# Performance work log

Hardware: AMD Instinct MI355X
Metric: run time of the kernel (lower is better)

## Reference

```python
import jax, jax.numpy as jnp
import numpy as np
from jax import lax

N, GH, GE, LH, LL = 19, 64, 64, 64, 2
B, T = 256, 256


def _normalized_adjacency(A):
    # A: (..., n, n). Add self-loops, symmetric degree normalization.
    n = A.shape[-1]
    A = A + jnp.eye(n, dtype=A.dtype)
    deg = jnp.clip(A.sum(axis=-1), 1e-6, None)  # (..., n)
    dis = deg ** -0.5
    return A * dis[..., :, None] * dis[..., None, :]


def _graph_encoder(A, w1_w, w1_b, w2_w, w2_b):
    # A: (B, T, n, n) -> (B, T, GE). Node features X = A rows.
    An = _normalized_adjacency(A)
    X = jax.nn.relu(An @ (A @ w1_w.T + w1_b))   # (B,T,n,GH)
    X = jax.nn.relu(An @ (X @ w2_w.T + w2_b))   # (B,T,n,GE)
    return X.mean(axis=-2)


def _lstm_layer(x, Wih, Whh, bih, bhh):
    # x: (B, T, D); PyTorch gate order i,f,g,o. Returns (B, T, H).
    Bb = x.shape[0]
    H = Whh.shape[1]
    xg = x @ Wih.T + (bih + bhh)  # precompute input contributions (B,T,4H)

    def step(carry, xt):
        h, c = carry
        gates = xt + h @ Whh.T
        i, f, g, o = jnp.split(gates, 4, axis=-1)
        c = jax.nn.sigmoid(f) * c + jax.nn.sigmoid(i) * jnp.tanh(g)
        h = jax.nn.sigmoid(o) * jnp.tanh(c)
        return (h, c), h

    h0 = jnp.zeros((Bb, H), x.dtype)
    (_, _), hs = lax.scan(step, (h0, h0), jnp.swapaxes(xg, 0, 1))
    return jnp.swapaxes(hs, 0, 1)


def setup_inputs() -> dict:
    key = jax.random.key(0)
    ks = jax.random.split(key, 20)
    s = 0.1
    inp = {
        'conn': jax.random.uniform(ks[0], (B, T, N, N), jnp.float32),
        'mask': jnp.ones((B, T), jnp.int32),
        'w1_w': jax.random.normal(ks[1], (GH, N), jnp.float32) * s,
        'w1_b': jax.random.normal(ks[2], (GH,), jnp.float32) * s,
        'w2_w': jax.random.normal(ks[3], (GE, GH), jnp.float32) * s,
        'w2_b': jax.random.normal(ks[4], (GE,), jnp.float32) * s,
        'lstm_Wih0': jax.random.normal(ks[5], (4 * LH, GE), jnp.float32) * s,
        'lstm_Whh0': jax.random.normal(ks[6], (4 * LH, LH), jnp.float32) * s,
        'lstm_bih0': jax.random.normal(ks[7], (4 * LH,), jnp.float32) * s,
        'lstm_bhh0': jax.random.normal(ks[8], (4 * LH,), jnp.float32) * s,
        'lstm_Wih1': jax.random.normal(ks[9], (4 * LH, LH), jnp.float32) * s,
        'lstm_Whh1': jax.random.normal(ks[10], (4 * LH, LH), jnp.float32) * s,
        'lstm_bih1': jax.random.normal(ks[11], (4 * LH,), jnp.float32) * s,
        'lstm_bhh1': jax.random.normal(ks[12], (4 * LH,), jnp.float32) * s,
        'fc1_w': jax.random.normal(ks[13], (32, LH), jnp.float32) * s,
        'fc1_b': jax.random.normal(ks[14], (32,), jnp.float32) * s,
        'fc2_w': jax.random.normal(ks[15], (2, 32), jnp.float32) * s,
        'fc2_b': jax.random.normal(ks[16], (2,), jnp.float32) * s,
    }
    return inp


def reference(conn, mask, w1_w, w1_b, w2_w, w2_b,
              lstm_Wih0, lstm_Whh0, lstm_bih0, lstm_bhh0,
              lstm_Wih1, lstm_Whh1, lstm_bih1, lstm_bhh1,
              fc1_w, fc1_b, fc2_w, fc2_b):
    emb = _graph_encoder(conn, w1_w, w1_b, w2_w, w2_b)  # (B,T,GE)
    mf = mask.astype(emb.dtype)
    emb = emb * mf[:, :, None]
    out = _lstm_layer(emb, lstm_Wih0, lstm_Whh0, lstm_bih0, lstm_bhh0)
    out = _lstm_layer(out, lstm_Wih1, lstm_Whh1, lstm_bih1, lstm_bhh1)  # (B,T,LH)
    lengths = jnp.clip(mask.sum(axis=1), 1, None)
    last_idx = jnp.clip(lengths - 1, 0, None)  # (B,)
    last_h = jnp.take_along_axis(out, last_idx[:, None, None], axis=1)[:, 0, :]
    h = jax.nn.relu(last_h @ fc1_w.T + fc1_b)
    return h @ fc2_w.T + fc2_b  # (B,2) logits
```

## Files before the change

### kernel.cpp

```cpp
#include <hip/hip_runtime.h>
#include <hip/hip_bf16.h>
#include <math.h>

#define GN 19
#define BB 256
#define TT 256

typedef short short8 __attribute__((ext_vector_type(8)));
typedef float f4 __attribute__((ext_vector_type(4)));
typedef unsigned short u16;

union Frag { int i[4]; short8 s; };

#define LWAIT() __asm__ volatile("s_waitcnt lgkmcnt(0)" ::: "memory")
#define WGBAR() __asm__ volatile("s_waitcnt lgkmcnt(0)\ns_barrier" ::: "memory")
#define PIN8(x) __asm__ volatile("" : "+v"(x))
#define PINF(x) __asm__ volatile("" : "+v"(x))

#define MFMA(a,b,c) __builtin_amdgcn_mfma_f32_16x16x32_bf16(a,b,c,0,0,0)

__device__ __forceinline__ int pkbf(float a, float b) {
    __hip_bfloat162 h2 = __float22bfloat162_rn(make_float2(a, b));
    union { __hip_bfloat162 h; int i; } u; u.h = h2; return u.i;
}

__device__ __forceinline__ float fexp2(float x) { return __builtin_amdgcn_exp2f(x); }
__device__ __forceinline__ float frcp(float x)  { return __builtin_amdgcn_rcpf(x); }
__device__ __forceinline__ float sigm(float x)  { return frcp(1.f + fexp2(-1.4426950408889634f * x)); }
__device__ __forceinline__ float tanha(float x) { float e = fexp2(2.8853900817779268f * x); return 1.f - 2.f * frcp(e + 1.f); }

__global__ __launch_bounds__(64) void encoder_mfma(
    const float* __restrict__ conn,
    const int*   __restrict__ mask,
    const float* __restrict__ w1_w,
    const float* __restrict__ w1_b,
    const float* __restrict__ w2_w,
    const float* __restrict__ w2_b,
    u16* __restrict__ emb,
    int num_graphs)
{
    __shared__ float S[2304];
    __shared__ float dis[32];
    __shared__ float ps[256];

    const int t = threadIdx.x;
    const int l15 = t & 15;
    const int quad = t >> 4;

    float km[8];
    #pragma unroll
    for (int j = 0; j < 8; ++j) km[j] = (quad * 8 + j < GN) ? 1.f : 0.f;

    int rr[6], cc[6];
    #pragma unroll
    for (int i = 0; i < 6; ++i) {
        int e = t + 64 * i;
        rr[i] = e / GN;
        cc[i] = e - rr[i] * GN;
    }

    Frag w1F[4];
    #pragma unroll
    for (int nt = 0; nt < 4; ++nt) {
        int n = nt * 16 + l15;
        #pragma unroll
        for (int p = 0; p < 4; ++p) {
            int k0 = quad * 8 + 2 * p, k1 = k0 + 1;
            float a = (k0 < GN) ? w1_w[n * GN + k0] : 0.f;
            float b = (k1 < GN) ? w1_w[n * GN + k1] : 0.f;
            w1F[nt].i[p] = pkbf(a, b);
        }
    }
    Frag w2F[2][4];
    #pragma unroll
    for (int kt = 0; kt < 2; ++kt)
        #pragma unroll
        for (int nt = 0; nt < 4; ++nt) {
            int n = nt * 16 + l15;
            #pragma unroll
            for (int p = 0; p < 4; ++p) {
                int k = kt * 32 + quad * 8 + 2 * p;
                w2F[kt][nt].i[p] = pkbf(w2_w[n * 64 + k], w2_w[n * 64 + k + 1]);
            }
        }
    float b1v[4], b2v[4];
    #pragma unroll
    for (int nt = 0; nt < 4; ++nt) {
        b1v[nt] = w1_b[nt * 16 + l15];
        b2v[nt] = w2_b[nt * 16 + l15];
    }

    float pf[6];
    {
        int g0 = blockIdx.x < num_graphs ? blockIdx.x : 0;
        const float* Ag = conn + (size_t)g0 * (GN * GN);
        #pragma unroll
        for (int i = 0; i < 6; ++i) {
            int e = t + 64 * i;
            if (e < GN * GN) pf[i] = Ag[e];
        }
    }

    #pragma unroll 1
    for (int g = blockIdx.x; g < num_graphs; g += gridDim.x) {
        #pragma unroll
        for (int i = 0; i < 4; ++i) {
            int s = t + 64 * i;
            int row = s >> 3, c4 = s & 7;
            f4 z = {0.f, 0.f, 0.f, 0.f};
            *(f4*)&S[row * 68 + c4 * 4] = z;
        }
        LWAIT();
        #pragma unroll
        for (int i = 0; i < 6; ++i) {
            if (t + 64 * i < GN * GN) S[rr[i] * 68 + cc[i]] = pf[i];
        }
        {
            int gn = g + gridDim.x;
            const float* Ag = conn + (size_t)(gn < num_graphs ? gn : g) * (GN * GN);
            #pragma unroll
            for (int i = 0; i < 6; ++i) {
                int e = t + 64 * i;
                if (e < GN * GN) pf[i] = Ag[e];
            }
        }
        LWAIT();

        if (t < 32) {
            float dv = 0.f;
            if (t < GN) {
                float d = 1.0f;
                #pragma unroll
                for (int c4 = 0; c4 < 8; ++c4) {
                    f4 v = *(f4*)&S[t * 68 + c4 * 4];
                    d += v.x + v.y + v.z + v.w;
                }
                dv = rsqrtf(d);
            }
            dis[t] = dv;
        }
        LWAIT();

        float dk[8];
        {
            f4 v0 = *(f4*)&dis[quad * 8];
            f4 v1 = *(f4*)&dis[quad * 8 + 4];
            dk[0]=v0.x; dk[1]=v0.y; dk[2]=v0.z; dk[3]=v0.w;
            dk[4]=v1.x; dk[5]=v1.y; dk[6]=v1.z; dk[7]=v1.w;
        }
        Frag aF[2], anF[2];
        #pragma unroll
        for (int mt = 0; mt < 2; ++mt) {
            int m = l15 + 16 * mt;
            float dm = dis[m];
            f4 v0 = *(f4*)&S[m * 68 + quad * 8];
            f4 v1 = *(f4*)&S[m * 68 + quad * 8 + 4];
            float av[8] = {v0.x, v0.y, v0.z, v0.w, v1.x, v1.y, v1.z, v1.w};
            float an[8];
            #pragma unroll
            for (int j = 0; j < 8; ++j) {
                int k = quad * 8 + j;
                an[j] = (av[j] + (m == k ? 1.f : 0.f)) * dm * dk[j];
            }
            #pragma unroll
            for (int p = 0; p < 4; ++p) {
                aF[mt].i[p]  = pkbf(av[2*p], av[2*p+1]);
                anF[mt].i[p] = pkbf(an[2*p], an[2*p+1]);
            }
        }
        LWAIT();

        #pragma unroll
        for (int mt = 0; mt < 2; ++mt)
            #pragma unroll
            for (int nt = 0; nt < 4; ++nt) {
                float bb = b1v[nt];
                f4 c = {bb, bb, bb, bb};
                c = MFMA(aF[mt].s, w1F[nt].s, c);
                int col = nt * 16 + l15;
                #pragma unroll
                for (int r = 0; r < 4; ++r)
                    S[col * 36 + (mt * 16 + quad * 4 + r)] = c[r];
            }
        LWAIT();

        Frag hF[4];
        #pragma unroll
        for (int nt = 0; nt < 4; ++nt) {
            int n = nt * 16 + l15;
            f4 v0 = *(f4*)&S[n * 36 + quad * 8];
            f4 v1 = *(f4*)&S[n * 36 + quad * 8 + 4];
            float vv[8] = {v0.x, v0.y, v0.z, v0.w, v1.x, v1.y, v1.z, v1.w};
            #pragma unroll
            for (int p = 0; p < 4; ++p)
                hF[nt].i[p] = pkbf(vv[2*p] * km[2*p], vv[2*p+1] * km[2*p+1]);
        }
        LWAIT();

        #pragma unroll
        for (int mt = 0; mt < 2; ++mt)
            #pragma unroll
            for (int nt = 0; nt < 4; ++nt) {
                f4 c = {0.f, 0.f, 0.f, 0.f};
                c = MFMA(anF[mt].s, hF[nt].s, c);
                int col = nt * 16 + l15;
                #pragma unroll
                for (int r = 0; r < 4; ++r)
                    S[(mt * 16 + quad * 4 + r) * 68 + col] = fmaxf(c[r], 0.f);
            }
        LWAIT();

        Frag xF[2][2];
        #pragma unroll
        for (int mt = 0; mt < 2; ++mt) {
            int m = l15 + 16 * mt;
            #pragma unroll
            for (int kt = 0; kt < 2; ++kt) {
                f4 v0 = *(f4*)&S[m * 68 + kt * 32 + quad * 8];
                f4 v1 = *(f4*)&S[m * 68 + kt * 32 + quad * 8 + 4];
                xF[mt][kt].i[0] = pkbf(v0.x, v0.y);
                xF[mt][kt].i[1] = pkbf(v0.z, v0.w);
                xF[mt][kt].i[2] = pkbf(v1.x, v1.y);
                xF[mt][kt].i[3] = pkbf(v1.z, v1.w);
            }
        }
        LWAIT();

        #pragma unroll
        for (int mt = 0; mt < 2; ++mt)
            #pragma unroll
            for (int nt = 0; nt < 4; ++nt) {
                float bb = b2v[nt];
                f4 c = {bb, bb, bb, bb};
                c = MFMA(xF[mt][0].s, w2F[0][nt].s, c);
                c = MFMA(xF[mt][1].s, w2F[1][nt].s, c);
                int col = nt * 16 + l15;
                #pragma unroll
                for (int r = 0; r < 4; ++r)
                    S[col * 36 + (mt * 16 + quad * 4 + r)] = c[r];
            }
        LWAIT();

        Frag hG[4];
        #pragma unroll
        for (int nt = 0; nt < 4; ++nt) {
            int n = nt * 16 + l15;
            f4 v0 = *(f4*)&S[n * 36 + quad * 8];
            f4 v1 = *(f4*)&S[n * 36 + quad * 8 + 4];
            float vv[8] = {v0.x, v0.y, v0.z, v0.w, v1.x, v1.y, v1.z, v1.w};
            #pragma unroll
            for (int p = 0; p < 4; ++p)
                hG[nt].i[p] = pkbf(vv[2*p] * km[2*p], vv[2*p+1] * km[2*p+1]);
        }

        float cs[4];
        #pragma unroll
        for (int nt = 0; nt < 4; ++nt) cs[nt] = 0.f;
        #pragma unroll
        for (int mt = 0; mt < 2; ++mt)
            #pragma unroll
            for (int nt = 0; nt < 4; ++nt) {
                f4 c = {0.f, 0.f, 0.f, 0.f};
                c = MFMA(anF[mt].s, hG[nt].s, c);
                if (mt == 0) {
                    cs[nt] += fmaxf(c[0], 0.f) + fmaxf(c[1], 0.f)
                            + fmaxf(c[2], 0.f) + fmaxf(c[3], 0.f);
                } else if (quad == 0) {
                    cs[nt] += fmaxf(c[0], 0.f) + fmaxf(c[1], 0.f) + fmaxf(c[2], 0.f);
                }
            }
        #pragma unroll
        for (int nt = 0; nt < 4; ++nt)
            ps[quad * 64 + nt * 16 + l15] = cs[nt];
        LWAIT();
        float tot = ps[t] + ps[64 + t] + ps[128 + t] + ps[192 + t];
        float mf = (float)mask[g];
        float v = tot * (1.f / 19.f) * mf;
        emb[(size_t)g * 64 + t] = (u16)(unsigned)pkbf(v, v);
        LWAIT();
    }
}

__device__ __forceinline__ void read_h1(const u16* __restrict__ hs,
                                        int off, Frag* __restrict__ BH)
{
    #pragma unroll
    for (int kt = 0; kt < 2; ++kt) {
        int4 vh = *(const int4*)&hs[off + kt * 32];
        BH[kt].i[0] = vh.x; BH[kt].i[1] = vh.y;
        BH[kt].i[2] = vh.z; BH[kt].i[3] = vh.w;
    }
}

__global__ __launch_bounds__(512) __attribute__((amdgpu_waves_per_eu(2, 2)))
void lstm_mfma(
    const u16*   __restrict__ x,
    const int*   __restrict__ mask,
    const float* __restrict__ Wih0, const float* __restrict__ Whh0,
    const float* __restrict__ bih0, const float* __restrict__ bhh0,
    const float* __restrict__ Wih1, const float* __restrict__ Whh1,
    const float* __restrict__ bih1, const float* __restrict__ bhh1,
    const float* __restrict__ fc1_w, const float* __restrict__ fc1_b,
    const float* __restrict__ fc2_w, const float* __restrict__ fc2_b,
    float* __restrict__ out)
{
    __shared__ __attribute__((aligned(16))) u16 h0s[2][16 * 72];
    __shared__ __attribute__((aligned(16))) u16 h1s[2][16 * 72];
    __shared__ float hlast[16][68];
    __shared__ float red[512];
    __shared__ int   li_s[16];

    const int tid  = threadIdx.x;
    const int w    = tid >> 6;
    const int grp  = w >> 2;
    const int wl   = w & 3;
    const int lane = tid & 63;
    const int l15  = lane & 15;
    const int quad = lane >> 4;
    const int bb0  = blockIdx.x * 16;

    for (int i = tid; i < 16 * 72; i += 512) h1s[0][i] = 0;

    {
        int b16 = tid >> 5, j = tid & 31;
        int s = 0;
        #pragma unroll
        for (int c8 = 0; c8 < 8; ++c8)
            s += mask[(bb0 + b16) * TT + j + 32 * c8];
        red[tid] = (float)s;
    }
    __syncthreads();
    if (tid < 16) {
        float s = 0.f;
        #pragma unroll
        for (int j = 0; j < 32; ++j) s += red[tid * 32 + j];
        int li = (int)s - 1;
        li_s[tid] = li < 0 ? 0 : (li > TT - 1 ? TT - 1 : li);
    }
    __syncthreads();
    const int li = li_s[l15];

    const float* __restrict__ Wx = grp ? Wih1 : Wih0;
    const float* __restrict__ Wh = grp ? Whh1 : Whh0;
    const float* __restrict__ bi = grp ? bih1 : bih0;
    const float* __restrict__ bh = grp ? bhh1 : bhh0;

    Frag Ax[4][2], Ah[4][2];
    f4 biasv[4];
    #pragma unroll
    for (int mt = 0; mt < 4; ++mt) {
        int mg = 4 * wl + mt;
        int orig = (l15 & 3) * 64 + (mg * 4 + (l15 >> 2));
        #pragma unroll
        for (int kt = 0; kt < 2; ++kt)
            #pragma unroll
            for (int p = 0; p < 4; ++p) {
                int k = kt * 32 + quad * 8 + 2 * p;
                Ax[mt][kt].i[p] = pkbf(Wx[orig * 64 + k], Wx[orig * 64 + k + 1]);
                Ah[mt][kt].i[p] = pkbf(Wh[orig * 64 + k], Wh[orig * 64 + k + 1]);
            }
        int uu = mg * 4 + quad;
        #pragma unroll
        for (int r = 0; r < 4; ++r)
            biasv[mt][r] = bi[r * 64 + uu] + bh[r * 64 + uu];
    }
    #pragma unroll
    for (int mt = 0; mt < 4; ++mt) {
        PIN8(Ax[mt][0].s); PIN8(Ax[mt][1].s);
        PIN8(Ah[mt][0].s); PIN8(Ah[mt][1].s);
        PINF(biasv[mt]);
    }

    const int ubase = 16 * wl + quad;
    const int hoff = l15 * 72 + quad * 8;

    Frag BH0[2], BH1[2], BXn[2];
    #pragma unroll
    for (int kt = 0; kt < 2; ++kt)
        #pragma unroll
        for (int p = 0; p < 4; ++p) {
            BXn[kt].i[p] = 0; BH0[kt].i[p] = 0; BH1[kt].i[p] = 0;
        }
    float cst[4] = {0.f, 0.f, 0.f, 0.f};
    float hlv[4] = {0.f, 0.f, 0.f, 0.f};

    const u16* __restrict__ xb = x + (size_t)(bb0 + l15) * TT * 64;
    if (grp == 0) {
        BXn[0] = *(const Frag*)&xb[quad * 8];
        BXn[1] = *(const Frag*)&xb[32 + quad * 8];
    }

    #pragma unroll 1
    for (int it = 0; it <= TT; ++it) {
        const int cur = it & 1;
        f4 g[4];
        bool act = false;

        if (grp == 0) {
            if (it < TT) {
                act = true;
                Frag bx0 = BXn[0], bx1 = BXn[1];
                int tn = it + 1 < TT ? it + 1 : TT - 1;
                BXn[0] = *(const Frag*)&xb[(size_t)tn * 64 + quad * 8];
                BXn[1] = *(const Frag*)&xb[(size_t)tn * 64 + 32 + quad * 8];

                #pragma unroll
                for (int mt = 0; mt < 4; ++mt) {
                    f4 ca = biasv[mt];
                    ca = MFMA(Ax[mt][0].s, bx0.s,    ca);
                    ca = MFMA(Ah[mt][0].s, BH0[0].s, ca);
                    f4 cb = {0.f, 0.f, 0.f, 0.f};
                    cb = MFMA(Ax[mt][1].s, bx1.s,    cb);
                    cb = MFMA(Ah[mt][1].s, BH0[1].s, cb);
                    g[mt] = ca + cb;
                }
            }
        } else {
            if (it >= 1) {
                act = true;
                #pragma unroll
                for (int mt = 0; mt < 4; ++mt) {
                    f4 ca = biasv[mt];
                    ca = MFMA(Ax[mt][0].s, BH0[0].s, ca);
                    ca = MFMA(Ah[mt][0].s, BH1[0].s, ca);
                    f4 cb = {0.f, 0.f, 0.f, 0.f};
                    cb = MFMA(Ax[mt][1].s, BH0[1].s, cb);
                    cb = MFMA(Ah[mt][1].s, BH1[1].s, cb);
                    g[mt] = ca + cb;
                }
            }
        }

        if (act) {
            u16* __restrict__ dst = grp ? h1s[cur] : h0s[cur];
            #pragma unroll
            for (int mt = 0; mt < 4; ++mt) {
                f4 gg = g[mt];
                float si = sigm(gg[0]), sf = sigm(gg[1]);
                float tg = tanha(gg[2]), so = sigm(gg[3]);
                float cc = fmaf(sf, cst[mt], si * tg);
                cst[mt] = cc;
                float h = so * tanha(cc);
                if (grp && it - 1 == li) hlv[mt] = h;
                dst[l15 * 72 + ubase + 4 * mt] = (u16)(unsigned)pkbf(h, h);
            }
        }

        WGBAR();

        if (it < TT) {
            read_h1(h0s[cur], hoff, BH0);
            if (grp) read_h1(h1s[cur], hoff, BH1);
        }
    }

    if (grp == 1) {
        #pragma unroll
        for (int mt = 0; mt < 4; ++mt)
            hlast[l15][ubase + 4 * mt] = hlv[mt];
    }
    __syncthreads();
    {
        int b = tid >> 5, o = tid & 31;
        float acc = fc1_b[o];
        const float* fw = fc1_w + o * 64;
        #pragma unroll
        for (int j = 0; j < 64; ++j)
            acc = fmaf(hlast[b][j], fw[j], acc);
        red[b * 32 + o] = fmaxf(acc, 0.f);
    }
    __syncthreads();
    if (tid < 32) {
        int b = tid >> 1, o = tid & 1;
        float acc = fc2_b[o];
        #pragma unroll
        for (int j = 0; j < 32; ++j)
            acc = fmaf(fc2_w[o * 32 + j], red[b * 32 + j], acc);
        out[(bb0 + b) * 2 + o] = acc;
    }
}

extern "C" void kernel_launch(void* const* d_in, const int* in_sizes, int n_in,
                              void* d_out, int out_size, void* d_ws, size_t ws_size,
                              hipStream_t stream)
{
    const float* conn  = (const float*)d_in[0];
    const int*   mask  = (const int*)  d_in[1];
    const float* w1_w  = (const float*)d_in[2];
    const float* w1_b  = (const float*)d_in[3];
    const float* w2_w  = (const float*)d_in[4];
    const float* w2_b  = (const float*)d_in[5];
    const float* Wih0  = (const float*)d_in[6];
    const float* Whh0  = (const float*)d_in[7];
    const float* bih0  = (const float*)d_in[8];
    const float* bhh0  = (const float*)d_in[9];
    const float* Wih1  = (const float*)d_in[10];
    const float* Whh1  = (const float*)d_in[11];
    const float* bih1  = (const float*)d_in[12];
    const float* bhh1  = (const float*)d_in[13];
    const float* fc1_w = (const float*)d_in[14];
    const float* fc1_b = (const float*)d_in[15];
    const float* fc2_w = (const float*)d_in[16];
    const float* fc2_b = (const float*)d_in[17];

    float* out = (float*)d_out;
    u16*   emb = (u16*)d_ws;

    const int num_graphs = BB * TT;

    encoder_mfma<<<8192, 64, 0, stream>>>(
        conn, mask, w1_w, w1_b, w2_w, w2_b, emb, num_graphs);

    lstm_mfma<<<16, 512, 0, stream>>>(
        emb, mask, Wih0, Whh0, bih0, bhh0, Wih1, Whh1, bih1, bhh1,
        fc1_w, fc1_b, fc2_w, fc2_b, out);
}
```

Measured before the change: 539.9 us.

## Pack four graph waves per encoder block with shared bf16 weight fragments

The encoder now runs 256-thread blocks with four independent waves, each handling its own graph stream, and keeps the pre-packed bf16 weight fragments in LDS instead of per-thread registers. Intermediate activations are stored in LDS as bf16 with a smaller per-wave footprint, so the pack/convert steps between MFMAs disappear. The final mean reduction uses cross-lane shuffles instead of an LDS scratch buffer. The intent is to cut register pressure and LDS use, raise occupancy and reduce LDS traffic, at the cost of extra LDS reads of weights on every graph.

```diff
diff --git a/kernel.cpp b/kernel.cpp
--- a/kernel.cpp
+++ b/kernel.cpp
@@ -23,13 +23,17 @@
     __hip_bfloat162 h2 = __float22bfloat162_rn(make_float2(a, b));
     union { __hip_bfloat162 h; int i; } u; u.h = h2; return u.i;
 }
+__device__ __forceinline__ u16 bf16of(float v) {
+    return (u16)(unsigned)pkbf(v, v);
+}
 
 __device__ __forceinline__ float fexp2(float x) { return __builtin_amdgcn_exp2f(x); }
 __device__ __forceinline__ float frcp(float x)  { return __builtin_amdgcn_rcpf(x); }
 __device__ __forceinline__ float sigm(float x)  { return frcp(1.f + fexp2(-1.4426950408889634f * x)); }
 __device__ __forceinline__ float tanha(float x) { float e = fexp2(2.8853900817779268f * x); return 1.f - 2.f * frcp(e + 1.f); }
 
-__global__ __launch_bounds__(64) void encoder_mfma(
+__global__ __launch_bounds__(256) __attribute__((amdgpu_waves_per_eu(2, 4)))
+void encoder_mfma(
     const float* __restrict__ conn,
     const int*   __restrict__ mask,
     const float* __restrict__ w1_w,
@@ -39,17 +43,56 @@
     u16* __restrict__ emb,
     int num_graphs)
 {
-    __shared__ float S[2304];
-    __shared__ float dis[32];
-    __shared__ float ps[256];
-
-    const int t = threadIdx.x;
+    __shared__ __attribute__((aligned(16))) float SA[4][1280];
+    __shared__ __attribute__((aligned(16))) u16  wb[12][64][8];
+    __shared__ float dis4[4][32];
+
+    const int tid = threadIdx.x;
+    const int tw  = tid >> 6;
+    const int t   = tid & 63;
     const int l15 = t & 15;
     const int quad = t >> 4;
 
-    float km[8];
+    if (tw == 0) {
+        #pragma unroll
+        for (int nt = 0; nt < 4; ++nt) {
+            int n = nt * 16 + l15;
+            Frag f;
+            #pragma unroll
+            for (int p = 0; p < 4; ++p) {
+                int k0 = quad * 8 + 2 * p, k1 = k0 + 1;
+                float a = (k0 < GN) ? w1_w[n * GN + k0] : 0.f;
+                float b = (k1 < GN) ? w1_w[n * GN + k1] : 0.f;
+                f.i[p] = pkbf(a, b);
+            }
+            *(int4*)&wb[nt][t][0] = *(int4*)&f;
+        }
+        #pragma unroll
+        for (int kt = 0; kt < 2; ++kt)
+            #pragma unroll
+            for (int nt = 0; nt < 4; ++nt) {
+                int n = nt * 16 + l15;
+                Frag f;
+                #pragma unroll
+                for (int p = 0; p < 4; ++p) {
+                    int k = kt * 32 + quad * 8 + 2 * p;
+                    f.i[p] = pkbf(w2_w[n * 64 + k], w2_w[n * 64 + k + 1]);
+                }
+                *(int4*)&wb[4 + kt * 4 + nt][t][0] = *(int4*)&f;
+            }
+    }
+    float b1v[4], b2v[4];
     #pragma unroll
-    for (int j = 0; j < 8; ++j) km[j] = (quad * 8 + j < GN) ? 1.f : 0.f;
+    for (int nt = 0; nt < 4; ++nt) {
+        b1v[nt] = w1_b[nt * 16 + l15];
+        b2v[nt] = w2_b[nt * 16 + l15];
+    }
+    __syncthreads();
+
+    float* __restrict__ S   = SA[tw];
+    u16*  __restrict__ SH   = (u16*)S;
+    u16*  __restrict__ SX   = (u16*)S;
+    float* __restrict__ dis = dis4[tw];
 
     int rr[6], cc[6];
     #pragma unroll
@@ -59,40 +102,9 @@
         cc[i] = e - rr[i] * GN;
     }
 
-    Frag w1F[4];
-    #pragma unroll
-    for (int nt = 0; nt < 4; ++nt) {
-        int n = nt * 16 + l15;
-        #pragma unroll
-        for (int p = 0; p < 4; ++p) {
-            int k0 = quad * 8 + 2 * p, k1 = k0 + 1;
-            float a = (k0 < GN) ? w1_w[n * GN + k0] : 0.f;
-            float b = (k1 < GN) ? w1_w[n * GN + k1] : 0.f;
-            w1F[nt].i[p] = pkbf(a, b);
-        }
-    }
-    Frag w2F[2][4];
-    #pragma unroll
-    for (int kt = 0; kt < 2; ++kt)
-        #pragma unroll
-        for (int nt = 0; nt < 4; ++nt) {
-            int n = nt * 16 + l15;
-            #pragma unroll
-            for (int p = 0; p < 4; ++p) {
-                int k = kt * 32 + quad * 8 + 2 * p;
-                w2F[kt][nt].i[p] = pkbf(w2_w[n * 64 + k], w2_w[n * 64 + k + 1]);
-            }
-        }
-    float b1v[4], b2v[4];
-    #pragma unroll
-    for (int nt = 0; nt < 4; ++nt) {
-        b1v[nt] = w1_b[nt * 16 + l15];
-        b2v[nt] = w2_b[nt * 16 + l15];
-    }
-
     float pf[6];
     {
-        int g0 = blockIdx.x < num_graphs ? blockIdx.x : 0;
+        int g0 = blockIdx.x * 4 + tw;
         const float* Ag = conn + (size_t)g0 * (GN * GN);
         #pragma unroll
         for (int i = 0; i < 6; ++i) {
@@ -102,21 +114,21 @@
     }
 
     #pragma unroll 1
-    for (int g = blockIdx.x; g < num_graphs; g += gridDim.x) {
+    for (int g = blockIdx.x * 4 + tw; g < num_graphs; g += gridDim.x * 4) {
         #pragma unroll
         for (int i = 0; i < 4; ++i) {
             int s = t + 64 * i;
             int row = s >> 3, c4 = s & 7;
             f4 z = {0.f, 0.f, 0.f, 0.f};
-            *(f4*)&S[row * 68 + c4 * 4] = z;
+            *(f4*)&S[row * 36 + c4 * 4] = z;
         }
         LWAIT();
         #pragma unroll
         for (int i = 0; i < 6; ++i) {
-            if (t + 64 * i < GN * GN) S[rr[i] * 68 + cc[i]] = pf[i];
+            if (t + 64 * i < GN * GN) S[rr[i] * 36 + cc[i]] = pf[i];
         }
         {
-            int gn = g + gridDim.x;
+            int gn = g + gridDim.x * 4;
             const float* Ag = conn + (size_t)(gn < num_graphs ? gn : g) * (GN * GN);
             #pragma unroll
             for (int i = 0; i < 6; ++i) {
@@ -132,7 +144,7 @@
                 float d = 1.0f;
                 #pragma unroll
                 for (int c4 = 0; c4 < 8; ++c4) {
-                    f4 v = *(f4*)&S[t * 68 + c4 * 4];
+                    f4 v = *(f4*)&S[t * 36 + c4 * 4];
                     d += v.x + v.y + v.z + v.w;
                 }
                 dv = rsqrtf(d);
@@ -153,8 +165,8 @@
         for (int mt = 0; mt < 2; ++mt) {
             int m = l15 + 16 * mt;
             float dm = dis[m];
-            f4 v0 = *(f4*)&S[m * 68 + quad * 8];
-            f4 v1 = *(f4*)&S[m * 68 + quad * 8 + 4];
+            f4 v0 = *(f4*)&S[m * 36 + quad * 8];
+            f4 v1 = *(f4*)&S[m * 36 + quad * 8 + 4];
             float av[8] = {v0.x, v0.y, v0.z, v0.w, v1.x, v1.y, v1.z, v1.w};
             float an[8];
             #pragma unroll
@@ -171,43 +183,45 @@
         LWAIT();
 
         #pragma unroll
-        for (int mt = 0; mt < 2; ++mt)
-            #pragma unroll
-            for (int nt = 0; nt < 4; ++nt) {
+        for (int nt = 0; nt < 4; ++nt) {
+            Frag wf; *(int4*)&wf = *(int4*)&wb[nt][t][0];
+            int nn = nt * 16 + l15;
+            #pragma unroll
+            for (int mt = 0; mt < 2; ++mt) {
                 float bb = b1v[nt];
                 f4 c = {bb, bb, bb, bb};
-                c = MFMA(aF[mt].s, w1F[nt].s, c);
-                int col = nt * 16 + l15;
-                #pragma unroll
-                for (int r = 0; r < 4; ++r)
-                    S[col * 36 + (mt * 16 + quad * 4 + r)] = c[r];
-            }
+                c = MFMA(aF[mt].s, wf.s, c);
+                #pragma unroll
+                for (int r = 0; r < 4; ++r) {
+                    int k = mt * 16 + quad * 4 + r;
+                    float vv = c[r];
+                    if (mt == 1) vv = (quad == 0 && r < 3) ? vv : 0.f;
+                    SH[nn * 40 + k] = bf16of(vv);
+                }
+            }
+        }
         LWAIT();
 
         Frag hF[4];
         #pragma unroll
+        for (int nt = 0; nt < 4; ++nt)
+            *(int4*)&hF[nt] = *(const int4*)&SH[(nt * 16 + l15) * 40 + quad * 8];
+        LWAIT();
+
+        #pragma unroll
         for (int nt = 0; nt < 4; ++nt) {
-            int n = nt * 16 + l15;
-            f4 v0 = *(f4*)&S[n * 36 + quad * 8];
-            f4 v1 = *(f4*)&S[n * 36 + quad * 8 + 4];
-            float vv[8] = {v0.x, v0.y, v0.z, v0.w, v1.x, v1.y, v1.z, v1.w};
-            #pragma unroll
-            for (int p = 0; p < 4; ++p)
-                hF[nt].i[p] = pkbf(vv[2*p] * km[2*p], vv[2*p+1] * km[2*p+1]);
-        }
-        LWAIT();
-
-        #pragma unroll
-        for (int mt = 0; mt < 2; ++mt)
-            #pragma unroll
-            for (int nt = 0; nt < 4; ++nt) {
+            int nn = nt * 16 + l15;
+            #pragma unroll
+            for (int mt = 0; mt < 2; ++mt) {
                 f4 c = {0.f, 0.f, 0.f, 0.f};
                 c = MFMA(anF[mt].s, hF[nt].s, c);
-                int col = nt * 16 + l15;
-                #pragma unroll
-                for (int r = 0; r < 4; ++r)
-                    S[(mt * 16 + quad * 4 + r) * 68 + col] = fmaxf(c[r], 0.f);
-            }
+                #pragma unroll
+                for (int r = 0; r < 4; ++r) {
+                    int m = mt * 16 + quad * 4 + r;
+                    SX[m * 40 + nn] = bf16of(fmaxf(c[r], 0.f));
+                }
+            }
+        }
         LWAIT();
 
         Frag xF[2][2];
@@ -215,68 +229,63 @@
         for (int mt = 0; mt < 2; ++mt) {
             int m = l15 + 16 * mt;
             #pragma unroll
-            for (int kt = 0; kt < 2; ++kt) {
-                f4 v0 = *(f4*)&S[m * 68 + kt * 32 + quad * 8];
-                f4 v1 = *(f4*)&S[m * 68 + kt * 32 + quad * 8 + 4];
-                xF[mt][kt].i[0] = pkbf(v0.x, v0.y);
-                xF[mt][kt].i[1] = pkbf(v0.z, v0.w);
-                xF[mt][kt].i[2] = pkbf(v1.x, v1.y);
-                xF[mt][kt].i[3] = pkbf(v1.z, v1.w);
-            }
-        }
-        LWAIT();
-
-        #pragma unroll
-        for (int mt = 0; mt < 2; ++mt)
-            #pragma unroll
-            for (int nt = 0; nt < 4; ++nt) {
+            for (int kt = 0; kt < 2; ++kt)
+                *(int4*)&xF[mt][kt] = *(const int4*)&SX[m * 40 + kt * 32 + quad * 8];
+        }
+        LWAIT();
+
+        #pragma unroll
+        for (int nt = 0; nt < 4; ++nt) {
+            Frag w20; *(int4*)&w20 = *(int4*)&wb[4 + nt][t][0];
+            Frag w21; *(int4*)&w21 = *(int4*)&wb[8 + nt][t][0];
+            int nn = nt * 16 + l15;
+            #pragma unroll
+            for (int mt = 0; mt < 2; ++mt) {
                 float bb = b2v[nt];
                 f4 c = {bb, bb, bb, bb};
-                c = MFMA(xF[mt][0].s, w2F[0][nt].s, c);
-                c = MFMA(xF[mt][1].s, w2F[1][nt].s, c);
-                int col = nt * 16 + l15;
-                #pragma unroll
-                for (int r = 0; r < 4; ++r)
-                    S[col * 36 + (mt * 16 + quad * 4 + r)] = c[r];
-            }
-        LWAIT();
-
-        Frag hG[4];
+                c = MFMA(xF[mt][0].s, w20.s, c);
+                c = MFMA(xF[mt][1].s, w21.s, c);
+                #pragma unroll
+                for (int r = 0; r < 4; ++r) {
+                    int k = mt * 16 + quad * 4 + r;
+                    float vv = c[r];
+                    if (mt == 1) vv = (quad == 0 && r < 3) ? vv : 0.f;
+                    SH[nn * 40 + k] = bf16of(vv);
+                }
+            }
+        }
+        LWAIT();
+
+        float cs[4];
         #pragma unroll
         for (int nt = 0; nt < 4; ++nt) {
-            int n = nt * 16 + l15;
-            f4 v0 = *(f4*)&S[n * 36 + quad * 8];
-            f4 v1 = *(f4*)&S[n * 36 + quad * 8 + 4];
-            float vv[8] = {v0.x, v0.y, v0.z, v0.w, v1.x, v1.y, v1.z, v1.w};
-            #pragma unroll
-            for (int p = 0; p < 4; ++p)
-                hG[nt].i[p] = pkbf(vv[2*p] * km[2*p], vv[2*p+1] * km[2*p+1]);
-        }
-
-        float cs[4];
-        #pragma unroll
-        for (int nt = 0; nt < 4; ++nt) cs[nt] = 0.f;
-        #pragma unroll
-        for (int mt = 0; mt < 2; ++mt)
-            #pragma unroll
-            for (int nt = 0; nt < 4; ++nt) {
+            Frag hG; *(int4*)&hG = *(const int4*)&SH[(nt * 16 + l15) * 40 + quad * 8];
+            float acc = 0.f;
+            #pragma unroll
+            for (int mt = 0; mt < 2; ++mt) {
                 f4 c = {0.f, 0.f, 0.f, 0.f};
-                c = MFMA(anF[mt].s, hG[nt].s, c);
+                c = MFMA(anF[mt].s, hG.s, c);
                 if (mt == 0) {
-                    cs[nt] += fmaxf(c[0], 0.f) + fmaxf(c[1], 0.f)
-                            + fmaxf(c[2], 0.f) + fmaxf(c[3], 0.f);
+                    acc += fmaxf(c[0], 0.f) + fmaxf(c[1], 0.f)
+                         + fmaxf(c[2], 0.f) + fmaxf(c[3], 0.f);
                 } else if (quad == 0) {
-                    cs[nt] += fmaxf(c[0], 0.f) + fmaxf(c[1], 0.f) + fmaxf(c[2], 0.f);
-                }
-            }
-        #pragma unroll
-        for (int nt = 0; nt < 4; ++nt)
-            ps[quad * 64 + nt * 16 + l15] = cs[nt];
-        LWAIT();
-        float tot = ps[t] + ps[64 + t] + ps[128 + t] + ps[192 + t];
+                    acc += fmaxf(c[0], 0.f) + fmaxf(c[1], 0.f) + fmaxf(c[2], 0.f);
+                }
+            }
+            cs[nt] = acc;
+        }
+        #pragma unroll
+        for (int nt = 0; nt < 4; ++nt) {
+            cs[nt] += __shfl_xor(cs[nt], 16);
+            cs[nt] += __shfl_xor(cs[nt], 32);
+        }
+        float tot = cs[0];
+        tot = (quad == 1) ? cs[1] : tot;
+        tot = (quad == 2) ? cs[2] : tot;
+        tot = (quad == 3) ? cs[3] : tot;
         float mf = (float)mask[g];
         float v = tot * (1.f / 19.f) * mf;
-        emb[(size_t)g * 64 + t] = (u16)(unsigned)pkbf(v, v);
+        emb[(size_t)g * 64 + t] = bf16of(v);
         LWAIT();
     }
 }
@@ -508,7 +517,7 @@
 
     const int num_graphs = BB * TT;
 
-    encoder_mfma<<<8192, 64, 0, stream>>>(
+    encoder_mfma<<<2048, 256, 0, stream>>>(
         conn, mask, w1_w, w1_b, w2_w, w2_b, emb, num_graphs);
 
     lstm_mfma<<<16, 512, 0, stream>>>(
```

Result: faster. 499.8 us (-7.4%).
